# Performance work log

Measured on AMD Instinct MI355X. Metric: run time of the kernel, lower is better.

Reference implementation:

```python
import jax, jax.numpy as jnp
import numpy as np
import math

B_SZ, D_IN, D_OUT, Q, K = 256, 512, 64, 4, 4


def setup_inputs() -> dict:
    key = jax.random.key(0)
    k0, k1, k2, k3, k4, k5, k6 = jax.random.split(key, 7)
    X0 = jax.random.normal(k0, (B_SZ, D_IN), dtype=jnp.float32)
    t = jax.random.normal(k1, (B_SZ,), dtype=jnp.float32)
    # nn.Linear(D_in, Q): weight [Q, D_in], bias [Q]
    Wc_w = jax.random.normal(k2, (Q, D_IN), dtype=jnp.float32) / np.sqrt(D_IN)
    Wc_b = jax.random.normal(k3, (Q,), dtype=jnp.float32) / np.sqrt(D_IN)
    w = jax.random.normal(k4, (Q,), dtype=jnp.float32)
    A = jax.random.normal(k5, (D_OUT, Q, K), dtype=jnp.float32) / math.sqrt(Q * K)
    Bp = jax.random.uniform(k6, (D_OUT, Q, K), dtype=jnp.float32) * (2.0 * math.pi)
    return {"X0": X0, "t": t, "Wc_w": Wc_w, "Wc_b": Wc_b, "w": w, "A": A, "Bp": Bp}


def reference(X0, t, Wc_w, Wc_b, w, A, Bp):
    k_vec = jnp.arange(1, K + 1, dtype=X0.dtype)          # [K]
    C = X0 @ Wc_w.T + Wc_b                                 # [B, Q]
    t2 = t[:, None]                                        # [B, 1]
    time_term = (w[None, :] * t2)[:, None, :]              # [B, 1, Q]
    # Faithful to the torch code: [B,Q] + [B,1,Q] broadcasts to [B, B, Q]
    angle = C + time_term                                  # [B, B, Q]
    angle_k = angle[..., None] * k_vec                     # [B, B, Q, K]
    inner = angle_k[:, :, None, :, :] + Bp                 # [B, B, D_out, Q, K]
    V = jnp.sum(A * jnp.sin(inner), axis=(3, 4))           # [B, B, D_out]
    return V
```

## Files before the change

kernel.cpp:

```cpp
#include <hip/hip_runtime.h>
#include <math.h>

#define BSZ   256
#define DIN   512
#define DOUT  64
#define NQK   16


__global__ __launch_bounds__(256) void prep_kernel(
    const float* __restrict__ X0, const float* __restrict__ t,
    const float* __restrict__ Wc_w, const float* __restrict__ Wc_b,
    const float* __restrict__ w, const float* __restrict__ A,
    const float* __restrict__ Bp, float* __restrict__ ws)
{
    float* SJ = ws;
    float* CJ = ws + 4096;
    float* SI = ws + 8192;
    float* CI = ws + 12288;
    float* AP = ws + 16384;
    float* BQ = ws + 17408;

    const int j    = blockIdx.x;
    const int tid  = threadIdx.x;
    const int lane = tid & 63;
    const int q    = tid >> 6;

    if (tid < 16) {
        const int qq = tid >> 2;
        const int kk = (tid & 3) + 1;
        float arg = w[qq] * t[j] * (float)kk;
        float s, c;
        sincosf(arg, &s, &c);
        SI[j * 16 + tid] = s;
        CI[j * 16 + tid] = c;
    }

    if (j < DOUT && tid >= 64 && tid < 80) {
        const int qk = tid - 64;
        float a = A[j * 16 + qk];
        float b = Bp[j * 16 + qk];
        float sb, cb;
        sincosf(b, &sb, &cb);
        AP[j * 16 + qk] = a * cb;
        BQ[j * 16 + qk] = a * sb;
    }

    const float* xrow = X0 + (size_t)j * DIN;
    const float* wrow = Wc_w + (size_t)q * DIN;
    float part = 0.f;
#pragma unroll
    for (int m = 0; m < DIN / 64; ++m)
        part += xrow[lane + 64 * m] * wrow[lane + 64 * m];
#pragma unroll
    for (int off = 32; off > 0; off >>= 1)
        part += __shfl_xor(part, off, 64);
    float cval = part + Wc_b[q];

    if (lane < 4) {
        float arg = cval * (float)(lane + 1);
        float s, c;
        sincosf(arg, &s, &c);
        SJ[j * 16 + q * 4 + lane] = s;
        CJ[j * 16 + q * 4 + lane] = c;
    }
}

__global__ __launch_bounds__(256) void main_kernel(
    const float* __restrict__ ws, float* __restrict__ out)
{
    const float* SJ = ws;
    const float* CJ = ws + 4096;
    const float* SI = ws + 8192;
    const float* CI = ws + 12288;
    const float* AP = ws + 16384;
    const float* BQ = ws + 17408;

    const int b   = blockIdx.x;
    const int i   = b >> 2;
    const int jb0 = (b & 3) * 64;
    const int tid = threadIdx.x;
    const int o   = tid & 63;
    const int wv  = __builtin_amdgcn_readfirstlane(tid >> 6);
    const int jbase = jb0 + wv * 16;

    float ap[NQK], bq[NQK];
    {
        const float4* a4 = (const float4*)(AP + o * NQK);
        const float4* b4 = (const float4*)(BQ + o * NQK);
#pragma unroll
        for (int m = 0; m < 4; ++m) {
            float4 va = a4[m], vb = b4[m];
            ap[4 * m + 0] = va.x; ap[4 * m + 1] = va.y;
            ap[4 * m + 2] = va.z; ap[4 * m + 3] = va.w;
            bq[4 * m + 0] = vb.x; bq[4 * m + 1] = vb.y;
            bq[4 * m + 2] = vb.z; bq[4 * m + 3] = vb.w;
        }
    }

    float P[NQK], Qc[NQK];
#pragma unroll
    for (int qk = 0; qk < NQK; ++qk) {
        float si = SI[i * NQK + qk];
        float ci = CI[i * NQK + qk];
        P[qk]  = ap[qk] * ci - bq[qk] * si;
        Qc[qk] = ap[qk] * si + bq[qk] * ci;
    }

    float* outb = out + ((size_t)(i * 256 + jbase)) * 64 + o;

#pragma unroll 4
    for (int jj = 0; jj < 16; ++jj) {
        const float4* sj4 = (const float4*)(SJ + (jbase + jj) * NQK);
        const float4* cj4 = (const float4*)(CJ + (jbase + jj) * NQK);
        float acc = 0.f;
#pragma unroll
        for (int m = 0; m < 4; ++m) {
            float4 vs = sj4[m], vc = cj4[m];
            acc += P[4 * m + 0] * vs.x + Qc[4 * m + 0] * vc.x;
            acc += P[4 * m + 1] * vs.y + Qc[4 * m + 1] * vc.y;
            acc += P[4 * m + 2] * vs.z + Qc[4 * m + 2] * vc.z;
            acc += P[4 * m + 3] * vs.w + Qc[4 * m + 3] * vc.w;
        }
        outb[jj * 64] = acc;
    }
}

extern "C" void kernel_launch(void* const* d_in, const int* in_sizes, int n_in,
                              void* d_out, int out_size, void* d_ws, size_t ws_size,
                              hipStream_t stream) {
    const float* X0   = (const float*)d_in[0];
    const float* t    = (const float*)d_in[1];
    const float* Wc_w = (const float*)d_in[2];
    const float* Wc_b = (const float*)d_in[3];
    const float* w    = (const float*)d_in[4];
    const float* A    = (const float*)d_in[5];
    const float* Bp   = (const float*)d_in[6];
    float* out = (float*)d_out;
    float* ws  = (float*)d_ws;

    prep_kernel<<<dim3(BSZ), dim3(256), 0, stream>>>(X0, t, Wc_w, Wc_b, w, A, Bp, ws);
    main_kernel<<<dim3(1024), dim3(256), 0, stream>>>(ws, out);
}
```

Measured before the change: 78.80 us.

## Fuse prep and main kernels, recomputing projections per block in shared memory

Replaces the two-kernel pipeline with one kernel where each block computes all C projections and their sin/cos into shared memory, then produces one output row i. This removes the second launch and the global workspace round-trip. In exchange, every block redundantly recomputes the full X0·Wc product with strided, uncoalesced loads, which adds a large serial prologue before any output is written.

```diff
diff --git a/kernel.cpp b/kernel.cpp
--- a/kernel.cpp
+++ b/kernel.cpp
@@ -1,117 +1,77 @@
 #include <hip/hip_runtime.h>
 #include <math.h>
 
-#define BSZ   256
-#define DIN   512
-#define DOUT  64
-#define NQK   16
+#define NQK 16
 
-
-__global__ __launch_bounds__(256) void prep_kernel(
+__global__ __launch_bounds__(512) void fused_kernel(
     const float* __restrict__ X0, const float* __restrict__ t,
     const float* __restrict__ Wc_w, const float* __restrict__ Wc_b,
     const float* __restrict__ w, const float* __restrict__ A,
-    const float* __restrict__ Bp, float* __restrict__ ws)
+    const float* __restrict__ Bp, float* __restrict__ out)
 {
-    float* SJ = ws;
-    float* CJ = ws + 4096;
-    float* SI = ws + 8192;
-    float* CI = ws + 12288;
-    float* AP = ws + 16384;
-    float* BQ = ws + 17408;
+    __shared__ float SJ[256 * NQK];
+    __shared__ float CJ[256 * NQK];
 
-    const int j    = blockIdx.x;
-    const int tid  = threadIdx.x;
-    const int lane = tid & 63;
-    const int q    = tid >> 6;
-
-    if (tid < 16) {
-        const int qq = tid >> 2;
-        const int kk = (tid & 3) + 1;
-        float arg = w[qq] * t[j] * (float)kk;
-        float s, c;
-        sincosf(arg, &s, &c);
-        SI[j * 16 + tid] = s;
-        CI[j * 16 + tid] = c;
-    }
-
-    if (j < DOUT && tid >= 64 && tid < 80) {
-        const int qk = tid - 64;
-        float a = A[j * 16 + qk];
-        float b = Bp[j * 16 + qk];
-        float sb, cb;
-        sincosf(b, &sb, &cb);
-        AP[j * 16 + qk] = a * cb;
-        BQ[j * 16 + qk] = a * sb;
-    }
-
-    const float* xrow = X0 + (size_t)j * DIN;
-    const float* wrow = Wc_w + (size_t)q * DIN;
-    float part = 0.f;
-#pragma unroll
-    for (int m = 0; m < DIN / 64; ++m)
-        part += xrow[lane + 64 * m] * wrow[lane + 64 * m];
-#pragma unroll
-    for (int off = 32; off > 0; off >>= 1)
-        part += __shfl_xor(part, off, 64);
-    float cval = part + Wc_b[q];
-
-    if (lane < 4) {
-        float arg = cval * (float)(lane + 1);
-        float s, c;
-        sincosf(arg, &s, &c);
-        SJ[j * 16 + q * 4 + lane] = s;
-        CJ[j * 16 + q * 4 + lane] = c;
-    }
-}
-
-__global__ __launch_bounds__(256) void main_kernel(
-    const float* __restrict__ ws, float* __restrict__ out)
-{
-    const float* SJ = ws;
-    const float* CJ = ws + 4096;
-    const float* SI = ws + 8192;
-    const float* CI = ws + 12288;
-    const float* AP = ws + 16384;
-    const float* BQ = ws + 17408;
-
-    const int b   = blockIdx.x;
-    const int i   = b >> 2;
-    const int jb0 = (b & 3) * 64;
+    const int i   = blockIdx.x;
     const int tid = threadIdx.x;
     const int o   = tid & 63;
-    const int wv  = __builtin_amdgcn_readfirstlane(tid >> 6);
-    const int jbase = jb0 + wv * 16;
+    const int wv  = tid >> 6;
 
-    float ap[NQK], bq[NQK];
     {
-        const float4* a4 = (const float4*)(AP + o * NQK);
-        const float4* b4 = (const float4*)(BQ + o * NQK);
+        const int j  = tid >> 1;
+        const int q0 = (tid & 1) * 2;
+        const float4* xr  = (const float4*)(X0 + (size_t)j * 512);
+        const float4* wr0 = (const float4*)(Wc_w + (size_t)q0 * 512);
+        const float4* wr1 = (const float4*)(Wc_w + (size_t)(q0 + 1) * 512);
+        float acc0 = 0.f, acc1 = 0.f;
+#pragma unroll 4
+        for (int m = 0; m < 128; ++m) {
+            float4 a = xr[m], b0 = wr0[m], b1 = wr1[m];
+            acc0 += a.x * b0.x + a.y * b0.y + a.z * b0.z + a.w * b0.w;
+            acc1 += a.x * b1.x + a.y * b1.y + a.z * b1.z + a.w * b1.w;
+        }
+        const float c0 = acc0 + Wc_b[q0];
+        const float c1 = acc1 + Wc_b[q0 + 1];
 #pragma unroll
-        for (int m = 0; m < 4; ++m) {
-            float4 va = a4[m], vb = b4[m];
-            ap[4 * m + 0] = va.x; ap[4 * m + 1] = va.y;
-            ap[4 * m + 2] = va.z; ap[4 * m + 3] = va.w;
-            bq[4 * m + 0] = vb.x; bq[4 * m + 1] = vb.y;
-            bq[4 * m + 2] = vb.z; bq[4 * m + 3] = vb.w;
+        for (int k = 1; k <= 4; ++k) {
+            float s, c;
+            sincosf(c0 * (float)k, &s, &c);
+            SJ[j * NQK + q0 * 4 + (k - 1)] = s;
+            CJ[j * NQK + q0 * 4 + (k - 1)] = c;
+            sincosf(c1 * (float)k, &s, &c);
+            SJ[j * NQK + (q0 + 1) * 4 + (k - 1)] = s;
+            CJ[j * NQK + (q0 + 1) * 4 + (k - 1)] = c;
         }
     }
 
     float P[NQK], Qc[NQK];
+    {
+        const float ti = t[i];
 #pragma unroll
-    for (int qk = 0; qk < NQK; ++qk) {
-        float si = SI[i * NQK + qk];
-        float ci = CI[i * NQK + qk];
-        P[qk]  = ap[qk] * ci - bq[qk] * si;
-        Qc[qk] = ap[qk] * si + bq[qk] * ci;
+        for (int q = 0; q < 4; ++q) {
+            const float wt = w[q] * ti;
+#pragma unroll
+            for (int k = 1; k <= 4; ++k) {
+                const int qk = q * 4 + (k - 1);
+                float si, ci, sb, cb;
+                sincosf(wt * (float)k, &si, &ci);
+                float a = A[o * NQK + qk];
+                sincosf(Bp[o * NQK + qk], &sb, &cb);
+                const float ap = a * cb, bq = a * sb;
+                P[qk]  = ap * ci - bq * si;
+                Qc[qk] = ap * si + bq * ci;
+            }
+        }
     }
 
-    float* outb = out + ((size_t)(i * 256 + jbase)) * 64 + o;
+    __syncthreads();
 
-#pragma unroll 4
-    for (int jj = 0; jj < 16; ++jj) {
-        const float4* sj4 = (const float4*)(SJ + (jbase + jj) * NQK);
-        const float4* cj4 = (const float4*)(CJ + (jbase + jj) * NQK);
+    float* outb = out + (((size_t)i * 256) + (size_t)wv * 32) * 64 + o;
+#pragma unroll 2
+    for (int jj = 0; jj < 32; ++jj) {
+        const int j = wv * 32 + jj;
+        const float4* sj4 = (const float4*)(SJ + j * NQK);
+        const float4* cj4 = (const float4*)(CJ + j * NQK);
         float acc = 0.f;
 #pragma unroll
         for (int m = 0; m < 4; ++m) {
@@ -136,8 +96,7 @@
     const float* A    = (const float*)d_in[5];
     const float* Bp   = (const float*)d_in[6];
     float* out = (float*)d_out;
-    float* ws  = (float*)d_ws;
 
-    prep_kernel<<<dim3(BSZ), dim3(256), 0, stream>>>(X0, t, Wc_w, Wc_b, w, A, Bp, ws);
-    main_kernel<<<dim3(1024), dim3(256), 0, stream>>>(ws, out);
+    fused_kernel<<<dim3(256), dim3(512), 0, stream>>>(
+        X0, t, Wc_w, Wc_b, w, A, Bp, out);
 }
```

After: 129.0 us. 1.64x slower.
